# Performance work log

Measured on AMD Instinct MI355X. Metric: run time of the kernel, lower is better.

Reference implementation:

```python
import jax, jax.numpy as jnp
import numpy as np

EMBED = 2048
HEADS = 16
HEAD_DIM = EMBED // HEADS
CHUNK = 128
BASE = 10000.0
EPS = 1e-6


def setup_inputs() -> dict:
    key = jax.random.key(0)
    ks = jax.random.split(key, 8)
    b, n, d = 2, 2048, EMBED
    std = 0.02
    return {
        "x": jax.random.normal(ks[0], (b, n, d), jnp.float32),
        "Wq": jax.random.normal(ks[1], (d, d), jnp.float32) * std,
        "Wk": jax.random.normal(ks[2], (d, d), jnp.float32) * std,
        "Wv": jax.random.normal(ks[3], (d, d), jnp.float32) * std,
        "Wo": jax.random.normal(ks[4], (d, d), jnp.float32) * std,
        "Wg1": jax.random.normal(ks[5], (d, HEAD_DIM), jnp.float32) * std,
        "Wg2": jax.random.normal(ks[6], (HEAD_DIM, d), jnp.float32) * std,
        "norm_weight": jnp.ones((d,), jnp.float32),
    }


def _alibi_log_decay(h):
    # lightning attention 'constant' decay: per-head ALiBi slope, log_lambda = -slope
    slopes = 2.0 ** (-8.0 * (jnp.arange(h, dtype=jnp.float32) + 1.0) / h)
    return -slopes  # [h]


def _lrpe_rotate(x):
    # RoPE-like rotation on head_dim (half-split), offset=0
    b, n, h, d = x.shape
    half = d // 2
    theta = BASE ** (-2.0 * jnp.arange(half, dtype=jnp.float32) / d)  # [half]
    ang = jnp.arange(n, dtype=jnp.float32)[:, None] * theta[None, :]  # [n, half]
    cos = jnp.cos(ang)[None, :, None, :]
    sin = jnp.sin(ang)[None, :, None, :]
    x1, x2 = x[..., :half], x[..., half:]
    return jnp.concatenate([x1 * cos - x2 * sin, x1 * sin + x2 * cos], axis=-1)


def _lightning_attn(q, k, v, log_lam):
    # chunk-recurrent linear attention with per-head exponential decay
    b, n, h, d = q.shape
    C = CHUNK
    nc = n // C
    qc = q.reshape(b, nc, C, h, d).transpose(1, 0, 2, 3, 4)  # [nc,b,C,h,d]
    kc = k.reshape(b, nc, C, h, d).transpose(1, 0, 2, 3, 4)
    vc = v.reshape(b, nc, C, h, d).transpose(1, 0, 2, 3, 4)
    i = jnp.arange(C, dtype=jnp.float32)
    diff = i[:, None] - i[None, :]  # [C,C]
    # intra-chunk decay mask D[h,t,s] = lambda_h^(t-s) for t>=s else 0
    D = jnp.where(diff[None] >= 0, jnp.exp(log_lam[:, None, None] * diff[None]), 0.0)
    decay_q = jnp.exp(log_lam[None, :] * (i[:, None] + 1.0))    # [C,h]
    decay_k = jnp.exp(log_lam[None, :] * (C - 1.0 - i[:, None]))  # [C,h]
    lam_C = jnp.exp(log_lam * C)  # [h]

    def step(S, qkv):
        qi, ki, vi = qkv  # [b,C,h,d]
        scores = jnp.einsum('bthd,bshd->bhts', qi, ki) * D[None]
        o_intra = jnp.einsum('bhts,bshd->bthd', scores, vi)
        o_inter = jnp.einsum('bthd,bhde->bthe', qi * decay_q[None, :, :, None], S)
        S_new = lam_C[None, :, None, None] * S + jnp.einsum(
            'bshd,bshe->bhde', ki * decay_k[None, :, :, None], vi)
        return S_new, o_intra + o_inter

    S0 = jnp.zeros((b, h, d, d), q.dtype)
    _, o = jax.lax.scan(step, S0, (qc, kc, vc))  # o: [nc,b,C,h,d]
    return o.transpose(1, 0, 2, 3, 4).reshape(b, n, h, d)


def _gated_group_rmsnorm(o, gate, weight):
    # gate_pos='pre', gate_act='sigmoid', num_groups=HEADS
    b, n, d = o.shape
    x = o * jax.nn.sigmoid(gate)
    xg = x.reshape(b, n, HEADS, HEAD_DIM)
    ms = jnp.mean(xg * xg, axis=-1, keepdims=True)
    xg = xg * jax.lax.rsqrt(ms + EPS)
    return xg.reshape(b, n, d) * weight


def reference(x, Wq, Wk, Wv, Wo, Wg1, Wg2, norm_weight):
    b, n, d = x.shape
    q = (x @ Wq).reshape(b, n, HEADS, HEAD_DIM)
    k = (x @ Wk).reshape(b, n, HEADS, HEAD_DIM)
    v = (x @ Wv).reshape(b, n, HEADS, HEAD_DIM)
    q = jax.nn.silu(q)
    k = jax.nn.silu(k)
    q = _lrpe_rotate(q)
    k = _lrpe_rotate(k)
    log_lam = _alibi_log_decay(HEADS)
    o = _lightning_attn(q, k, v, log_lam).reshape(b, n, d)
    gate = (x @ Wg1) @ Wg2
    o = _gated_group_rmsnorm(o, gate, norm_weight)
    return o @ Wo
```

## Files before the change

### kernel.cpp

```cpp
#include <hip/hip_runtime.h>


#define DEV __device__ __forceinline__
typedef unsigned short u16;
typedef __bf16 bf16x8 __attribute__((ext_vector_type(8)));
typedef float f32x4 __attribute__((ext_vector_type(4)));
typedef u16 u16x8 __attribute__((ext_vector_type(8)));

DEV u16 f2bf(float f) {
  unsigned u = __builtin_bit_cast(unsigned, f);
  u += 0x7fffu + ((u >> 16) & 1u);
  return (u16)(u >> 16);
}
DEV float bf2f(u16 h) {
  unsigned u = ((unsigned)h) << 16;
  return __builtin_bit_cast(float, u);
}
DEV void async16(const u16* g, u16* l) {
  __builtin_amdgcn_global_load_lds(
      (const __attribute__((address_space(1))) unsigned int*)g,
      (__attribute__((address_space(3))) unsigned int*)l, 16, 0, 0);
}

__global__ void convert_f32_bf16(const float* __restrict__ in, u16* __restrict__ out, long n) {
  long i = ((long)blockIdx.x * blockDim.x + threadIdx.x) * 4;
  if (i >= n) return;
  float4 v = *(const float4*)(in + i);
  ushort4 p;
  p.x = f2bf(v.x); p.y = f2bf(v.y); p.z = f2bf(v.z); p.w = f2bf(v.w);
  *(ushort4*)(out + i) = p;
}

__global__ void transpose_all(const float* __restrict__ Wq, const float* __restrict__ Wk,
                              const float* __restrict__ Wv, const float* __restrict__ Wo,
                              const float* __restrict__ Wg1, const float* __restrict__ Wg2,
                              u16* __restrict__ wtqkvg, u16* __restrict__ wot,
                              u16* __restrict__ wg2t) {
  __shared__ float t[32][33];
  int id = blockIdx.x;
  const float* in; u16* out; int K, N, bx, by;
  bool perm = false;
  if (id < 12288) {
    int w = id >> 12, tt = id & 4095;
    in = (w == 0) ? Wq : (w == 1) ? Wk : Wv;
    out = wtqkvg + (long)w * 2048 * 2048;
    K = 2048; N = 2048; bx = tt & 63; by = tt >> 6;
    perm = (w < 2);
  } else if (id < 16384) {
    int tt = id - 12288;
    in = Wo; out = wot; K = 2048; N = 2048; bx = tt & 63; by = tt >> 6;
  } else if (id < 16640) {
    int tt = id - 16384;
    in = Wg1; out = wtqkvg + 6144L * 2048; K = 2048; N = 128; bx = tt & 3; by = tt >> 2;
  } else {
    int tt = id - 16640;
    in = Wg2; out = wg2t; K = 128; N = 2048; bx = tt & 63; by = tt >> 6;
  }
  int c = threadIdx.x & 31, r0 = threadIdx.x >> 5;
  for (int r = r0; r < 32; r += 8)
    t[r][c] = in[(long)(by * 32 + r) * N + bx * 32 + c];
  __syncthreads();
  for (int r = r0; r < 32; r += 8) {
    int n = bx * 32 + r, nr = n;
    if (perm) {
      int h = n >> 7, j = n & 127, jj = j & 63, hi = j >> 6;
      nr = h * 128 + (jj & 15) + 32 * (jj >> 4) + 16 * hi;
    }
    out[(long)nr * K + by * 32 + c] = f2bf(t[c][r]);
  }
}

template <typename OutT>
__global__ __launch_bounds__(256, 2) void gemm_bt(
    const u16* __restrict__ A, const u16* __restrict__ B, OutT* __restrict__ C,
    int M, int N, int K, int lda, int ldb, int ldc, int rot,
    int nc, long sA1, long sA2, long sB1, long sB2, long sC1, long sC2) {
  __shared__ u16 sA[128 * 32], sB[128 * 32];
  {
    int z = blockIdx.z, z1 = z / nc, z2 = z % nc;
    A += z1 * sA1 + z2 * sA2;
    B += z1 * sB1 + z2 * sB2;
    C += z1 * sC1 + z2 * sC2;
  }
  int bxs, bys;
  {
    int lin = blockIdx.x + gridDim.x * blockIdx.y;
    int per = 16 * gridDim.y;
    int g = lin / per, r = lin % per;
    int base = g * 16;
    int w = min(16, (int)gridDim.x - base);
    bxs = base + r % w; bys = r / w;
  }
  const int tid = threadIdx.x, lane = tid & 63, wid = tid >> 6;
  const int bm = bys * 128, bn = bxs * 128;
  const int ch0 = wid * 2, ch1 = ch0 + 1;
  const int lr = lane >> 2;
  const int ak = (((lane & 3) - ((lane >> 3) & 3)) & 3) * 8;
  const int ar0 = ch0 * 16 + lr, ar1 = ch1 * 16 + lr;
  const u16* gA0 = A + (long)(bm + ar0) * lda + ak;
  const u16* gA1 = A + (long)(bm + ar1) * lda + ak;
  const u16* gB0 = B + (long)(bn + ar0) * ldb + ak;
  const u16* gB1 = B + (long)(bn + ar1) * ldb + ak;
  u16* lA0 = sA + ch0 * 512; u16* lA1 = sA + ch1 * 512;
  u16* lB0 = sB + ch0 * 512; u16* lB1 = sB + ch1 * 512;
  const int wm = (wid & 1) * 64, wn = (wid >> 1) * 64;
  const int fm = lane & 15, kq = lane >> 4;
  const int qs = ((kq + (fm >> 1)) & 3) * 8;
  const int aoff = (wm >> 4) * 512 + fm * 32 + qs;
  const int boff = (wn >> 4) * 512 + fm * 32 + qs;
  f32x4 acc[4][4] = {};
  for (int kb = 0; kb < K; kb += 32) {
    async16(gA0, lA0); async16(gA1, lA1);
    async16(gB0, lB0); async16(gB1, lB1);
    gA0 += 32; gA1 += 32; gB0 += 32; gB1 += 32;
    __syncthreads();
    bf16x8 af[4], bfr[4];
#pragma unroll
    for (int i = 0; i < 4; i++) af[i] = *(const bf16x8*)&sA[aoff + i * 512];
#pragma unroll
    for (int i = 0; i < 4; i++) bfr[i] = *(const bf16x8*)&sB[boff + i * 512];
#pragma unroll
    for (int mt = 0; mt < 4; mt++)
#pragma unroll
      for (int nt = 0; nt < 4; nt++)
        acc[mt][nt] = __builtin_amdgcn_mfma_f32_16x16x32_bf16(af[mt], bfr[nt], acc[mt][nt], 0, 0, 0);
    __syncthreads();
  }
  const int cr = (lane >> 4) * 4;
  if constexpr (sizeof(OutT) == 2) {
    if (rot && bn < 4096) {
#pragma unroll
      for (int mt = 0; mt < 4; mt++)
#pragma unroll
        for (int r = 0; r < 4; r++) {
          long row = bm + wm + mt * 16 + cr + r;
          float tf = (float)(int)(row & 2047);
#pragma unroll
          for (int np = 0; np < 4; np += 2) {
            float x1 = acc[mt][np][r], x2 = acc[mt][np + 1][r];
            x1 = x1 / (1.f + __expf(-x1));
            x2 = x2 / (1.f + __expf(-x2));
            int jj = fm + 16 * ((wn >> 5) + (np >> 1));
            float th = exp2f(-13.287712379549449f * (float)jj * (1.f / 64.f));
            float sn, cs;
            sincosf(tf * th, &sn, &cs);
            C[row * ldc + bn + jj]      = f2bf(x1 * cs - x2 * sn);
            C[row * ldc + bn + 64 + jj] = f2bf(x1 * sn + x2 * cs);
          }
        }
      return;
    }
  }
#pragma unroll
  for (int mt = 0; mt < 4; mt++)
#pragma unroll
    for (int nt = 0; nt < 4; nt++)
#pragma unroll
      for (int r = 0; r < 4; r++) {
        long row = bm + wm + mt * 16 + cr + r;
        long col = bn + wn + nt * 16 + fm;
        float v = acc[mt][nt][r];
        if constexpr (sizeof(OutT) == 2) C[row * ldc + col] = f2bf(v);
        else                             C[row * ldc + col] = v;
      }
}

__global__ void transpose_kv(const u16* __restrict__ qkv, u16* __restrict__ kdT,
                             u16* __restrict__ vT) {
  __shared__ float t[32][33];
  int z = blockIdx.z, which = z >> 5, bh = z & 31;
  int b = bh >> 4, h = bh & 15;
  u16* out = which ? vT : kdT;
  int slab = which ? 2 : 1, decay = which ? 0 : 1;
  int n0 = blockIdx.x * 32, d0 = blockIdx.y * 32;
  int cc = threadIdx.x & 31, rr0 = threadIdx.x >> 5;
  float log_lam = -exp2f(-0.5f * (float)(h + 1));
  for (int rr = rr0; rr < 32; rr += 8) {
    int n = n0 + rr;
    float v = bf2f(qkv[(long)(b * 2048 + n) * 6272 + slab * 2048 + h * 128 + d0 + cc]);
    if (decay) v *= expf(log_lam * (float)(127 - (n & 127)));
    t[rr][cc] = v;
  }
  __syncthreads();
  for (int rr = rr0; rr < 32; rr += 8)
    out[((long)bh * 128 + d0 + rr) * 2048 + n0 + cc] = f2bf(t[cc][rr]);
}

__global__ void scan_state(const u16* __restrict__ U, u16* __restrict__ S_all) {
  int blk = blockIdx.x;
  int bh = blk >> 3, sl = blk & 7, h = bh & 15;
  float log_lam = -exp2f(-0.5f * (float)(h + 1));
  float lamC = expf(log_lam * 128.f);
  long off = (long)bh * 16 * 16384 + sl * 2048 + threadIdx.x * 8;
  float s[8];
#pragma unroll
  for (int j = 0; j < 8; j++) s[j] = 0.f;
  for (int c = 0; c < 16; c++) {
    long idx = off + (long)c * 16384;
    u16x8 sb;
#pragma unroll
    for (int j = 0; j < 8; j++) sb[j] = f2bf(s[j]);
    *(u16x8*)(S_all + idx) = sb;
    u16x8 ub = *(const u16x8*)(U + idx);
#pragma unroll
    for (int j = 0; j < 8; j++) s[j] = lamC * s[j] + bf2f(ub[j]);
  }
}

__global__ __launch_bounds__(256, 1) void attn_out(
    const u16* __restrict__ qkv, const u16* __restrict__ vT,
    const u16* __restrict__ S_all, const u16* __restrict__ gate,
    const float* __restrict__ nw, u16* __restrict__ nrm) {
  __shared__ u16 sA[128 * 32], sB[128 * 32], sK[128 * 32];
  __shared__ u16 sS[128 * 136];
  __shared__ float sNorm[2][128];
  const int blk = blockIdx.x;
  const int bh = blk >> 4, c = blk & 15;
  const int b = bh >> 4, h = bh & 15;
  const float log_lam = -exp2f(-0.5f * (float)(h + 1));
  const int tid = threadIdx.x, lane = tid & 63, wid = tid >> 6;
  const int wm = (wid & 1) * 64, wn = (wid >> 1) * 64;
  const int fm = lane & 15, fq = lane >> 4, kq = lane >> 4;
  const int lr = lane >> 2;
  const int ak = (((lane & 3) - ((lane >> 3) & 3)) & 3) * 8;
  const int ch0 = wid * 2, ch1 = ch0 + 1;
  const int r0 = ch0 * 16 + lr, r1 = ch1 * 16 + lr;
  const int qs = ((kq + (fm >> 1)) & 3) * 8;
  const int aoff = (wm >> 4) * 512 + fm * 32 + qs;
  const int boff = (wn >> 4) * 512 + fm * 32 + qs;
  const u16* qbase = qkv + (long)(b * 2048 + c * 128) * 6272 + h * 128;
  const u16* kbase = qbase + 2048;
  const u16* Sbase = S_all + ((long)bh * 16 + c) * 16384;
  const u16* vbase = vT + (long)bh * 262144 + (long)c * 128;

  f32x4 acc[4][4] = {};
  f32x4 sc[4][4] = {};
  for (int kb = 0; kb < 128; kb += 32) {
    async16(qbase + (long)r0 * 6272 + kb + ak, sA + ch0 * 512);
    async16(qbase + (long)r1 * 6272 + kb + ak, sA + ch1 * 512);
    async16(Sbase + r0 * 128 + kb + ak, sB + ch0 * 512);
    async16(Sbase + r1 * 128 + kb + ak, sB + ch1 * 512);
    async16(kbase + (long)r0 * 6272 + kb + ak, sK + ch0 * 512);
    async16(kbase + (long)r1 * 6272 + kb + ak, sK + ch1 * 512);
    __syncthreads();
    bf16x8 aq[4], bs[4], bk[4];
#pragma unroll
    for (int i = 0; i < 4; i++) {
      aq[i] = *(const bf16x8*)&sA[aoff + i * 512];
      bs[i] = *(const bf16x8*)&sB[boff + i * 512];
      bk[i] = *(const bf16x8*)&sK[boff + i * 512];
    }
#pragma unroll
    for (int mt = 0; mt < 4; mt++)
#pragma unroll
      for (int nt = 0; nt < 4; nt++) {
        acc[mt][nt] = __builtin_amdgcn_mfma_f32_16x16x32_bf16(aq[mt], bs[nt], acc[mt][nt], 0, 0, 0);
        sc[mt][nt] = __builtin_amdgcn_mfma_f32_16x16x32_bf16(aq[mt], bk[nt], sc[mt][nt], 0, 0, 0);
      }
    __syncthreads();
  }
#pragma unroll
  for (int mt = 0; mt < 4; mt++)
#pragma unroll
    for (int r = 0; r < 4; r++) {
      int t = wm + mt * 16 + fq * 4 + r;
      float d = expf(log_lam * (float)(t + 1));
#pragma unroll
      for (int nt = 0; nt < 4; nt++) acc[mt][nt][r] *= d;
    }
#pragma unroll
  for (int mt = 0; mt < 4; mt++)
#pragma unroll
    for (int nt = 0; nt < 4; nt++)
#pragma unroll
      for (int r = 0; r < 4; r++) {
        int t = wm + mt * 16 + fq * 4 + r;
        int s = wn + nt * 16 + fm;
        float v = sc[mt][nt][r];
        v = (t >= s) ? v * expf(log_lam * (float)(t - s)) : 0.f;
        sS[t * 136 + s] = f2bf(v);
      }
  __syncthreads();
  for (int kb = 0; kb < 128; kb += 32) {
    async16(vbase + r0 * 2048 + kb + ak, sB + ch0 * 512);
    async16(vbase + r1 * 2048 + kb + ak, sB + ch1 * 512);
    __syncthreads();
    bf16x8 as[4], bv[4];
#pragma unroll
    for (int i = 0; i < 4; i++) {
      as[i] = *(const bf16x8*)&sS[(wm + i * 16 + fm) * 136 + kb + kq * 8];
      bv[i] = *(const bf16x8*)&sB[boff + i * 512];
    }
#pragma unroll
    for (int mt = 0; mt < 4; mt++)
#pragma unroll
      for (int nt = 0; nt < 4; nt++)
        acc[mt][nt] = __builtin_amdgcn_mfma_f32_16x16x32_bf16(as[mt], bv[nt], acc[mt][nt], 0, 0, 0);
    __syncthreads();
  }
  const u16* gbase = gate + (long)(b * 2048 + c * 128) * 2048 + h * 128;
  float nwv[4];
#pragma unroll
  for (int nt = 0; nt < 4; nt++) nwv[nt] = nw[h * 128 + wn + nt * 16 + fm];
  float part[4][4];
#pragma unroll
  for (int mt = 0; mt < 4; mt++)
#pragma unroll
    for (int r = 0; r < 4; r++) {
      int t = wm + mt * 16 + fq * 4 + r;
      float p = 0.f;
#pragma unroll
      for (int nt = 0; nt < 4; nt++) {
        int e = wn + nt * 16 + fm;
        float g = bf2f(gbase[(long)t * 2048 + e]);
        float x = acc[mt][nt][r] / (1.f + __expf(-g));
        acc[mt][nt][r] = x;
        p += x * x;
      }
      part[mt][r] = p;
    }
#pragma unroll
  for (int o = 1; o < 16; o <<= 1)
#pragma unroll
    for (int mt = 0; mt < 4; mt++)
#pragma unroll
      for (int r = 0; r < 4; r++) part[mt][r] += __shfl_xor(part[mt][r], o);
  if (fm == 0) {
#pragma unroll
    for (int mt = 0; mt < 4; mt++)
#pragma unroll
      for (int r = 0; r < 4; r++)
        sNorm[wid >> 1][wm + mt * 16 + fq * 4 + r] = part[mt][r];
  }
  __syncthreads();
  long orow0 = (long)(b * 2048 + c * 128);
#pragma unroll
  for (int mt = 0; mt < 4; mt++)
#pragma unroll
    for (int r = 0; r < 4; r++) {
      int t = wm + mt * 16 + fq * 4 + r;
      float ms = (sNorm[0][t] + sNorm[1][t]) * (1.f / 128.f);
      float rs = rsqrtf(ms + 1e-6f);
#pragma unroll
      for (int nt = 0; nt < 4; nt++) {
        int e = wn + nt * 16 + fm;
        nrm[(orow0 + t) * 2048 + h * 128 + e] = f2bf(acc[mt][nt][r] * rs * nwv[nt]);
      }
    }
}

extern "C" void kernel_launch(void* const* d_in, const int* in_sizes, int n_in,
                              void* d_out, int out_size, void* d_ws, size_t ws_size,
                              hipStream_t stream) {
  (void)in_sizes; (void)n_in; (void)out_size; (void)ws_size;
  const float* x   = (const float*)d_in[0];
  const float* Wq  = (const float*)d_in[1];
  const float* Wk  = (const float*)d_in[2];
  const float* Wv  = (const float*)d_in[3];
  const float* Wo  = (const float*)d_in[4];
  const float* Wg1 = (const float*)d_in[5];
  const float* Wg2 = (const float*)d_in[6];
  const float* nw  = (const float*)d_in[7];
  float* out = (float*)d_out;

  char* ws = (char*)d_ws;
  size_t off = 0;
  auto alloc = [&](size_t bytes) -> void* {
    void* p = ws + off;
    off += (bytes + 255) & ~(size_t)255;
    return p;
  };
  u16* xb    = (u16*)alloc(4096UL * 2048 * 2);
  u16* wtqkv = (u16*)alloc(6272UL * 2048 * 2);
  u16* wot   = (u16*)alloc(2048UL * 2048 * 2);
  u16* wg2t  = (u16*)alloc(2048UL * 128 * 2);
  u16* qkvg  = (u16*)alloc(4096UL * 6272 * 2);
  u16* gate  = (u16*)alloc(4096UL * 2048 * 2);
  u16* kdT   = (u16*)alloc(32UL * 128 * 2048 * 2);
  u16* vT    = (u16*)alloc(32UL * 128 * 2048 * 2);
  u16* Ubuf  = (u16*)alloc(512UL * 16384 * 2);
  u16* S_all = (u16*)alloc(512UL * 16384 * 2);
  u16* nrm   = (u16*)alloc(4096UL * 2048 * 2);

  convert_f32_bf16<<<dim3(8192), dim3(256), 0, stream>>>(x, xb, 8388608L);
  transpose_all<<<dim3(16896), dim3(256), 0, stream>>>(Wq, Wk, Wv, Wo, Wg1, Wg2,
                                                       wtqkv, wot, wg2t);
  gemm_bt<u16><<<dim3(49, 32, 1), dim3(256), 0, stream>>>(xb, wtqkv, qkvg,
      4096, 6272, 2048, 2048, 2048, 6272, 1, 1, 0, 0, 0, 0, 0, 0);
  gemm_bt<u16><<<dim3(16, 32, 1), dim3(256), 0, stream>>>(qkvg + 6144, wg2t, gate,
      4096, 2048, 128, 6272, 128, 2048, 0, 1, 0, 0, 0, 0, 0, 0);
  transpose_kv<<<dim3(64, 4, 64), dim3(256), 0, stream>>>(qkvg, kdT, vT);
  gemm_bt<u16><<<dim3(1, 1, 512), dim3(256), 0, stream>>>(vT, kdT, Ubuf,
      128, 128, 128, 2048, 2048, 128, 0,
      16, 262144L, 128L, 262144L, 128L, 262144L, 16384L);
  scan_state<<<dim3(256), dim3(256), 0, stream>>>(Ubuf, S_all);
  attn_out<<<dim3(512), dim3(256), 0, stream>>>(qkvg, vT, S_all, gate, nw, nrm);
  gemm_bt<float><<<dim3(16, 32, 1), dim3(256), 0, stream>>>(nrm, wot, out,
      4096, 2048, 2048, 2048, 2048, 2048, 0, 1, 0, 0, 0, 0, 0, 0);
}
```

Measured before the change: 422.8 us.

## Add triple-buffered 128x256 GEMM kernel with tile swizzle for QKV and output projections

Introduces gemm_bt2, a 512-thread kernel that computes 128x256 tiles, keeps three LDS stages with async global-to-LDS loads two k-steps ahead, uses a single barrier per step, and raises wave priority around the MFMA block. Block indices are grouped in bands of 16 columns to improve L2 reuse. The QKV projection moves to this kernel, the leftover 128-column gate slice runs through the old kernel, and the output projection also uses the new kernel. The cost is an extra launch, larger tiles that produce fewer blocks for the output GEMM (256 blocks), and higher LDS and register use per block.

```diff
diff --git a/kernel.cpp b/kernel.cpp
--- a/kernel.cpp
+++ b/kernel.cpp
@@ -127,25 +127,111 @@
     __syncthreads();
   }
   const int cr = (lane >> 4) * 4;
+#pragma unroll
+  for (int mt = 0; mt < 4; mt++)
+#pragma unroll
+    for (int nt = 0; nt < 4; nt++)
+#pragma unroll
+      for (int r = 0; r < 4; r++) {
+        long row = bm + wm + mt * 16 + cr + r;
+        long col = bn + wn + nt * 16 + fm;
+        float v = acc[mt][nt][r];
+        if constexpr (sizeof(OutT) == 2) C[row * ldc + col] = f2bf(v);
+        else                             C[row * ldc + col] = v;
+      }
+}
+
+template <typename OutT>
+__global__ __launch_bounds__(512, 1) void gemm_bt2(
+    const u16* __restrict__ A, const u16* __restrict__ B, OutT* __restrict__ C,
+    int M, int N, int K, int lda, int ldb, int ldc, int rot) {
+  __shared__ u16 sA[3][128 * 32];
+  __shared__ u16 sB[3][256 * 32];
+  int bxs, bys;
+  {
+    int lin = blockIdx.x + gridDim.x * blockIdx.y;
+    int per = 16 * gridDim.y;
+    int g = lin / per, r = lin % per;
+    int base = g * 16;
+    int w = min(16, (int)gridDim.x - base);
+    bxs = base + r % w; bys = r / w;
+  }
+  const int tid = threadIdx.x, lane = tid & 63, wid = tid >> 6;
+  const int wr = wid & 1, wc = wid >> 1;
+  const int bm = bys * 128, bn = bxs * 256;
+  const int lr = lane >> 2;
+  const int ak = (((lane & 3) - ((lane >> 3) & 3)) & 3) * 8;
+  const u16* gA  = A + (long)(bm + wid * 16 + lr) * lda + ak;
+  const u16* gB0 = B + (long)(bn + wid * 32 + lr) * ldb + ak;
+  const u16* gB1 = gB0 + (long)16 * ldb;
+  u16* const baseA = (u16*)sA;
+  u16* const baseB = (u16*)sB;
+  const int fm = lane & 15, kq = lane >> 4;
+  const int qs = ((kq + (fm >> 1)) & 3) * 8;
+  const int aoff = (wr * 64 + fm) * 32 + qs;
+  const int boff = (wc * 64 + fm) * 32 + qs;
+  f32x4 acc[4][4] = {};
+  const int NT = K >> 5;
+  async16(gA, baseA + wid * 512);
+  async16(gB0, baseB + wid * 1024);
+  async16(gB1, baseB + wid * 1024 + 512);
+  async16(gA + 32, baseA + 4096 + wid * 512);
+  async16(gB0 + 32, baseB + 8192 + wid * 1024);
+  async16(gB1 + 32, baseB + 8192 + wid * 1024 + 512);
+  asm volatile("s_waitcnt vmcnt(3)" ::: "memory");
+  __builtin_amdgcn_s_barrier();
+  __builtin_amdgcn_sched_barrier(0);
+  int cur = 0;
+  for (int t = 0; t < NT; ++t) {
+    const u16* bufA = baseA + cur * 4096;
+    const u16* bufB = baseB + cur * 8192;
+    bf16x8 af[4], bfr[4];
+#pragma unroll
+    for (int i = 0; i < 4; i++) {
+      af[i]  = *(const bf16x8*)&bufA[aoff + i * 512];
+      bfr[i] = *(const bf16x8*)&bufB[boff + i * 512];
+    }
+    if (t + 2 < NT) {
+      int nxt = cur + 2; if (nxt >= 3) nxt -= 3;
+      long ko = (long)(t + 2) * 32;
+      async16(gA + ko, baseA + nxt * 4096 + wid * 512);
+      async16(gB0 + ko, baseB + nxt * 8192 + wid * 1024);
+      async16(gB1 + ko, baseB + nxt * 8192 + wid * 1024 + 512);
+    }
+    __builtin_amdgcn_s_setprio(1);
+#pragma unroll
+    for (int mt = 0; mt < 4; mt++)
+#pragma unroll
+      for (int nt = 0; nt < 4; nt++)
+        acc[mt][nt] = __builtin_amdgcn_mfma_f32_16x16x32_bf16(af[mt], bfr[nt], acc[mt][nt], 0, 0, 0);
+    __builtin_amdgcn_s_setprio(0);
+    if (t + 2 < NT) { asm volatile("s_waitcnt vmcnt(3)" ::: "memory"); }
+    else            { asm volatile("s_waitcnt vmcnt(0)" ::: "memory"); }
+    __builtin_amdgcn_s_barrier();
+    __builtin_amdgcn_sched_barrier(0);
+    cur = cur + 1; if (cur >= 3) cur = 0;
+  }
+  const int cr = kq * 4;
   if constexpr (sizeof(OutT) == 2) {
     if (rot && bn < 4096) {
 #pragma unroll
       for (int mt = 0; mt < 4; mt++)
 #pragma unroll
         for (int r = 0; r < 4; r++) {
-          long row = bm + wm + mt * 16 + cr + r;
+          long row = bm + wr * 64 + mt * 16 + cr + r;
           float tf = (float)(int)(row & 2047);
+          long hb = bn + (wc >> 1) * 128;
 #pragma unroll
           for (int np = 0; np < 4; np += 2) {
             float x1 = acc[mt][np][r], x2 = acc[mt][np + 1][r];
             x1 = x1 / (1.f + __expf(-x1));
             x2 = x2 / (1.f + __expf(-x2));
-            int jj = fm + 16 * ((wn >> 5) + (np >> 1));
+            int jj = fm + 16 * ((np >> 1) + 2 * (wc & 1));
             float th = exp2f(-13.287712379549449f * (float)jj * (1.f / 64.f));
             float sn, cs;
             sincosf(tf * th, &sn, &cs);
-            C[row * ldc + bn + jj]      = f2bf(x1 * cs - x2 * sn);
-            C[row * ldc + bn + 64 + jj] = f2bf(x1 * sn + x2 * cs);
+            C[row * ldc + hb + jj]      = f2bf(x1 * cs - x2 * sn);
+            C[row * ldc + hb + 64 + jj] = f2bf(x1 * sn + x2 * cs);
           }
         }
       return;
@@ -157,8 +243,8 @@
     for (int nt = 0; nt < 4; nt++)
 #pragma unroll
       for (int r = 0; r < 4; r++) {
-        long row = bm + wm + mt * 16 + cr + r;
-        long col = bn + wn + nt * 16 + fm;
+        long row = bm + wr * 64 + mt * 16 + cr + r;
+        long col = bn + wc * 64 + nt * 16 + fm;
         float v = acc[mt][nt][r];
         if constexpr (sizeof(OutT) == 2) C[row * ldc + col] = f2bf(v);
         else                             C[row * ldc + col] = v;
@@ -385,8 +471,10 @@
   convert_f32_bf16<<<dim3(8192), dim3(256), 0, stream>>>(x, xb, 8388608L);
   transpose_all<<<dim3(16896), dim3(256), 0, stream>>>(Wq, Wk, Wv, Wo, Wg1, Wg2,
                                                        wtqkv, wot, wg2t);
-  gemm_bt<u16><<<dim3(49, 32, 1), dim3(256), 0, stream>>>(xb, wtqkv, qkvg,
-      4096, 6272, 2048, 2048, 2048, 6272, 1, 1, 0, 0, 0, 0, 0, 0);
+  gemm_bt2<u16><<<dim3(24, 32, 1), dim3(512), 0, stream>>>(xb, wtqkv, qkvg,
+      4096, 6144, 2048, 2048, 2048, 6272, 1);
+  gemm_bt<u16><<<dim3(1, 32, 1), dim3(256), 0, stream>>>(xb, wtqkv + 6144L * 2048,
+      qkvg + 6144, 4096, 128, 2048, 2048, 2048, 6272, 0, 1, 0, 0, 0, 0, 0, 0);
   gemm_bt<u16><<<dim3(16, 32, 1), dim3(256), 0, stream>>>(qkvg + 6144, wg2t, gate,
       4096, 2048, 128, 6272, 128, 2048, 0, 1, 0, 0, 0, 0, 0, 0);
   transpose_kv<<<dim3(64, 4, 64), dim3(256), 0, stream>>>(qkvg, kdT, vT);
@@ -395,6 +483,6 @@
       16, 262144L, 128L, 262144L, 128L, 262144L, 16384L);
   scan_state<<<dim3(256), dim3(256), 0, stream>>>(Ubuf, S_all);
   attn_out<<<dim3(512), dim3(256), 0, stream>>>(qkvg, vT, S_all, gate, nw, nrm);
-  gemm_bt<float><<<dim3(16, 32, 1), dim3(256), 0, stream>>>(nrm, wot, out,
-      4096, 2048, 2048, 2048, 2048, 2048, 0, 1, 0, 0, 0, 0, 0, 0);
-}
+  gemm_bt2<float><<<dim3(8, 32, 1), dim3(512), 0, stream>>>(nrm, wot, out,
+      4096, 2048, 2048, 2048, 2048, 2048, 0);
+}
```

Result: slower. 477.6 us (+13.0%).
